# Performance work log

Hardware: AMD Instinct MI355X
Metric: run time of the kernel (lower is better)

The kernel has to match this reference:

```python
import jax, jax.numpy as jnp
import numpy as np

D_MODEL = 1024
N_HEADS = 16
D_HEAD = D_MODEL // N_HEADS


def setup_inputs() -> dict:
    key = jax.random.key(0)
    kx, kq, kk, kv, ko = jax.random.split(key, 5)
    s = 1.0 / np.sqrt(D_MODEL)  # ~ nn.Linear init scale
    return {
        "x": jax.random.normal(kx, (2, 2048, D_MODEL), dtype=jnp.float32),
        "Wq": jax.random.uniform(kq, (D_MODEL, D_MODEL), jnp.float32, -s, s),
        "Wk": jax.random.uniform(kk, (D_MODEL, D_MODEL), jnp.float32, -s, s),
        "Wv": jax.random.uniform(kv, (D_MODEL, D_MODEL), jnp.float32, -s, s),
        "Wo": jax.random.uniform(ko, (D_MODEL, D_MODEL), jnp.float32, -s, s),
    }


def reference(x, Wq, Wk, Wv, Wo):
    B, T, D = x.shape
    H, Dh = N_HEADS, D_HEAD
    # nn.Linear computes x @ W.T; project then split heads -> [B,H,T,Dh]
    q = (x @ Wq.T).reshape(B, T, H, Dh).transpose(0, 2, 1, 3)
    k = (x @ Wk.T).reshape(B, T, H, Dh).transpose(0, 2, 1, 3)
    v = (x @ Wv.T).reshape(B, T, H, Dh).transpose(0, 2, 1, 3)
    att = jnp.einsum("bhqd,bhkd->bhqk", q, k) / jnp.sqrt(jnp.float32(Dh))
    causal = jnp.tril(jnp.ones((T, T), dtype=bool))  # True = keep
    att = jnp.where(causal[None, None], att, -jnp.inf)
    w = jax.nn.softmax(att, axis=-1)
    out = jnp.einsum("bhqk,bhkd->bhqd", w, v)
    out = out.transpose(0, 2, 1, 3).reshape(B, T, D)
    return out @ Wo.T
```

## Files before the change

### kernel.cpp

```cpp
#include <hip/hip_runtime.h>
#include <hip/hip_bf16.h>

typedef __bf16 bf16;
typedef __bf16 bf16x4 __attribute__((ext_vector_type(4)));
typedef __bf16 bf16x8 __attribute__((ext_vector_type(8)));
typedef float  f32x4  __attribute__((ext_vector_type(4)));

#define DEV static __device__ __forceinline__

DEV void gload_lds16(const void* g, void* l) {
  __builtin_amdgcn_global_load_lds((const __attribute__((address_space(1))) void*)g,
                                   (__attribute__((address_space(3))) void*)l, 16, 0, 0);
}

DEV f32x4 mfma16(bf16x8 a, bf16x8 b, f32x4 c) {
  return __builtin_amdgcn_mfma_f32_16x16x32_bf16(a, b, c, 0, 0, 0);
}

__global__ void convert_all(const float* __restrict__ x,
                            const float* __restrict__ wq, const float* __restrict__ wk,
                            const float* __restrict__ wv, const float* __restrict__ wo,
                            bf16* __restrict__ xb,
                            bf16* __restrict__ wqb, bf16* __restrict__ wkb,
                            bf16* __restrict__ wvb, bf16* __restrict__ wob) {
  const int NX = 4194304;
  const int NW = 1048576;
  const int total4 = (NX + 4 * NW) / 4;
  for (int i = blockIdx.x * blockDim.x + threadIdx.x; i < total4;
       i += gridDim.x * blockDim.x) {
    int e = i * 4;
    const float* src; bf16* dst; int off;
    if (e < NX) { src = x; dst = xb; off = e; }
    else {
      int r = e - NX; int w = r >> 20; off = r & (NW - 1);
      src = (w == 0) ? wq : (w == 1) ? wk : (w == 2) ? wv : wo;
      dst = (w == 0) ? wqb : (w == 1) ? wkb : (w == 2) ? wvb : wob;
    }
    float4 v = *(const float4*)(src + off);
    bf16x4 o; o[0] = (bf16)v.x; o[1] = (bf16)v.y; o[2] = (bf16)v.z; o[3] = (bf16)v.w;
    *(bf16x4*)(dst + off) = o;
  }
}

__global__ __launch_bounds__(256) void gemm_qkv(const bf16* __restrict__ xb,
                                                const bf16* __restrict__ Wq_,
                                                const bf16* __restrict__ Wk_,
                                                const bf16* __restrict__ Wv_,
                                                bf16* __restrict__ Qg,
                                                bf16* __restrict__ Kg,
                                                bf16* __restrict__ Vtg) {
  const int z = blockIdx.z;
  const bf16* A  = (z == 2) ? Wv_ : xb;
  const bf16* Bw = (z == 0) ? Wq_ : (z == 1) ? Wk_ : xb;
  const int K = 1024;
  __shared__ bf16 As[128 * 32];
  __shared__ bf16 Bs[128 * 32];
  const int tid = threadIdx.x, w = tid >> 6, l = tid & 63;
  const int row0 = (z == 2 ? blockIdx.y : blockIdx.x) * 128;
  const int col0 = (z == 2 ? blockIdx.x : blockIdx.y) * 128;
  const int wr = (w >> 1) * 64, wc = (w & 1) * 64;
  const int lr = l & 15, lg = l >> 4;
  const int srow = l >> 2, scol = (l & 3) * 8;
  f32x4 acc[4][4] = {};

  for (int kt = 0; kt < 32; ++kt) {
    const int k0 = kt * 32;
#pragma unroll
    for (int i = 0; i < 2; ++i) {
      const int chunk = w * 2 + i;
      gload_lds16(A  + (row0 + chunk * 16 + srow) * K + k0 + scol, &As[chunk * 512]);
      gload_lds16(Bw + (col0 + chunk * 16 + srow) * K + k0 + scol, &Bs[chunk * 512]);
    }
    __syncthreads();
    bf16x8 af[4], bfr[4];
#pragma unroll
    for (int m = 0; m < 4; ++m) af[m]  = *(const bf16x8*)&As[(wr + m * 16 + lr) * 32 + lg * 8];
#pragma unroll
    for (int n = 0; n < 4; ++n) bfr[n] = *(const bf16x8*)&Bs[(wc + n * 16 + lr) * 32 + lg * 8];
#pragma unroll
    for (int m = 0; m < 4; ++m)
#pragma unroll
      for (int n = 0; n < 4; ++n)
        acc[m][n] = mfma16(af[m], bfr[n], acc[m][n]);
    __syncthreads();
  }

  if (z == 2) {
#pragma unroll
    for (int m = 0; m < 4; ++m)
#pragma unroll
      for (int n = 0; n < 4; ++n)
#pragma unroll
        for (int e = 0; e < 4; ++e) {
          const int rr = row0 + wr + m * 16 + lg * 4 + e;
          const int cc = col0 + wc + n * 16 + lr;
          const int h = rr >> 6, dh = rr & 63;
          const int b = cc >> 11, t = cc & 2047;
          Vtg[(((size_t)(b * 16 + h) * 64) + dh) * 2048 + t] = (bf16)acc[m][n][e];
        }
  } else {
    const float scl = (z == 0) ? 0.18033688011112042f : 1.0f;
    bf16* out = (z == 0) ? Qg : Kg;
#pragma unroll
    for (int m = 0; m < 4; ++m)
#pragma unroll
      for (int n = 0; n < 4; ++n)
#pragma unroll
        for (int e = 0; e < 4; ++e) {
          const int r = row0 + wr + m * 16 + lg * 4 + e;
          const int c = col0 + wc + n * 16 + lr;
          const int b = r >> 11, t = r & 2047;
          const int h = c >> 6,  dh = c & 63;
          out[(((size_t)(b * 16 + h) * 2048) + t) * 64 + dh] = (bf16)(acc[m][n][e] * scl);
        }
  }
}

__global__ __launch_bounds__(256) void attn(const bf16* __restrict__ Qg,
                                            const bf16* __restrict__ Kg,
                                            const bf16* __restrict__ Vtg,
                                            bf16* __restrict__ Obt) {
  const int bh = blockIdx.y;
  const int x  = blockIdx.x;
  const int tid = threadIdx.x, w = tid >> 6, l = tid & 63;
  const int lr = l & 15, lg = l >> 4;
  __shared__ bf16 Ks[2][4096];
  __shared__ bf16 Vs[2][4096];
  __shared__ bf16 Ps[4][1024];
  const size_t base = (size_t)bh * 2048 * 64;
  const char* kbase = (const char*)(Kg + base);
  const char* vbase = (const char*)(Vtg + base);

  const int rA0 = x * 64 + w * 16;
  const int rB0 = (31 - x) * 64 + w * 16;

  bf16x8 qA[2], qB[2];
  {
    const bf16* qp = Qg + base + (size_t)(rA0 + lr) * 64;
    qA[0] = *(const bf16x8*)(qp + lg * 8);
    qA[1] = *(const bf16x8*)(qp + 32 + lg * 8);
    const bf16* qq = Qg + base + (size_t)(rB0 + lr) * 64;
    qB[0] = *(const bf16x8*)(qq + lg * 8);
    qB[1] = *(const bf16x8*)(qq + 32 + lg * 8);
  }
  f32x4 oA[4] = {}, oB[4] = {};
  f32x4 lA = {}, lB = {};

  bf16x8 ones;
#pragma unroll
  for (int j = 0; j < 8; ++j) ones[j] = (bf16)1.0f;

  const int cxor = lr & 7;

  auto stage = [&](int kt, int buf) {
#pragma unroll
    for (int i = 0; i < 2; ++i) {
      const int p = (w * 2 + i) * 1024 + l * 16;
      const int sw = p ^ (((p >> 7) & 7) << 4);
      gload_lds16(kbase + (size_t)kt * 8192 + sw, &Ks[buf][(w * 2 + i) * 512]);
      const int vrow = p >> 7;
      const int vcol = (p & 127) ^ (((p >> 7) & 7) << 4);
      gload_lds16(vbase + (size_t)vrow * 4096 + kt * 128 + vcol,
                  &Vs[buf][(w * 2 + i) * 512]);
    }
  };

  auto computeTile = [&](int kt, int buf, int myrow0, bf16x8 (&qf)[2],
                         f32x4 (&acco)[4], f32x4& lacc) {
    const int k0 = kt * 64;
    const bool full = (k0 + 63 <= myrow0);
    f32x4 accs[4] = {};
    __builtin_amdgcn_s_setprio(1);
#pragma unroll
    for (int n = 0; n < 4; ++n) {
      const int r = n * 16 + lr;
      bf16x8 kf0 = *(const bf16x8*)&Ks[buf][(r * 128 + ((lg ^ cxor) << 4)) / 2];
      bf16x8 kf1 = *(const bf16x8*)&Ks[buf][(r * 128 + (((4 + lg) ^ cxor) << 4)) / 2];
      accs[n] = mfma16(kf0, qf[0], accs[n]);
      accs[n] = mfma16(kf1, qf[1], accs[n]);
    }
    __builtin_amdgcn_s_setprio(0);
    if (!full) {
      const int q = myrow0 + lr;
#pragma unroll
      for (int n = 0; n < 4; ++n) {
        const int keyb = k0 + n * 16 + lg * 4;
#pragma unroll
        for (int e = 0; e < 4; ++e)
          if (keyb + e > q) accs[n][e] = -__builtin_inff();
      }
    }
#pragma unroll
    for (int n = 0; n < 4; ++n)
#pragma unroll
      for (int e = 0; e < 4; ++e) accs[n][e] = exp2f(accs[n][e]);
#pragma unroll
    for (int n = 0; n < 4; ++n) {
      bf16x4 p4;
#pragma unroll
      for (int e = 0; e < 4; ++e) p4[e] = (bf16)accs[n][e];
      const int off = (lr * 128 + (n * 16 + lg * 4) * 2) ^ ((lr & 7) << 4);
      *(bf16x4*)((char*)Ps[w] + off) = p4;
    }
    __builtin_amdgcn_s_setprio(1);
#pragma unroll
    for (int c = 0; c < 2; ++c) {
      bf16x8 pf = *(const bf16x8*)((char*)Ps[w] +
                    (lr * 128 + (((c * 4 + lg) ^ cxor) << 4)));
      lacc = mfma16(pf, ones, lacc);
#pragma unroll
      for (int n = 0; n < 4; ++n) {
        const int r = n * 16 + lr;
        bf16x8 vf = *(const bf16x8*)&Vs[buf][(r * 128 + (((c * 4 + lg) ^ cxor) << 4)) / 2];
        acco[n] = mfma16(pf, vf, acco[n]);
      }
    }
    __builtin_amdgcn_s_setprio(0);
  };

  const int nkt = 32 - x;
  stage(0, 0);
  int cur = 0;
  for (int kt = 0; kt < nkt; ++kt) {
    __syncthreads();
    if (kt + 1 < nkt) stage(kt + 1, cur ^ 1);
    if (kt <= x)
      computeTile(kt, cur, rA0, qA, oA, lA);
    computeTile(kt, cur, rB0, qB, oB, lB);
    cur ^= 1;
  }

  const int b = bh >> 4, h = bh & 15;
  f32x4 invA, invB;
#pragma unroll
  for (int e = 0; e < 4; ++e) {
    invA[e] = __builtin_amdgcn_rcpf(lA[e]);
    invB[e] = __builtin_amdgcn_rcpf(lB[e]);
  }
#pragma unroll
  for (int n = 0; n < 4; ++n)
#pragma unroll
    for (int e = 0; e < 4; ++e) {
      const int rA = rA0 + lg * 4 + e;
      Obt[((size_t)(b * 2048 + rA)) * 1024 + h * 64 + n * 16 + lr] = (bf16)(oA[n][e] * invA[e]);
      const int rB = rB0 + lg * 4 + e;
      Obt[((size_t)(b * 2048 + rB)) * 1024 + h * 64 + n * 16 + lr] = (bf16)(oB[n][e] * invB[e]);
    }
}

__global__ __launch_bounds__(256) void gemm_out(const bf16* __restrict__ A,
                                                const bf16* __restrict__ Bw,
                                                float* __restrict__ Cout) {
  const int K = 1024;
  __shared__ bf16 As[128 * 32];
  __shared__ bf16 Bs[128 * 32];
  const int tid = threadIdx.x, w = tid >> 6, l = tid & 63;
  const int row0 = blockIdx.x * 128, col0 = blockIdx.y * 128;
  const int wr = (w >> 1) * 64, wc = (w & 1) * 64;
  const int lr = l & 15, lg = l >> 4;
  const int srow = l >> 2, scol = (l & 3) * 8;
  f32x4 acc[4][4] = {};

  for (int kt = 0; kt < 32; ++kt) {
    const int k0 = kt * 32;
#pragma unroll
    for (int i = 0; i < 2; ++i) {
      const int chunk = w * 2 + i;
      gload_lds16(A  + (row0 + chunk * 16 + srow) * K + k0 + scol, &As[chunk * 512]);
      gload_lds16(Bw + (col0 + chunk * 16 + srow) * K + k0 + scol, &Bs[chunk * 512]);
    }
    __syncthreads();
    bf16x8 af[4], bfr[4];
#pragma unroll
    for (int m = 0; m < 4; ++m) af[m]  = *(const bf16x8*)&As[(wr + m * 16 + lr) * 32 + lg * 8];
#pragma unroll
    for (int n = 0; n < 4; ++n) bfr[n] = *(const bf16x8*)&Bs[(wc + n * 16 + lr) * 32 + lg * 8];
#pragma unroll
    for (int m = 0; m < 4; ++m)
#pragma unroll
      for (int n = 0; n < 4; ++n)
        acc[m][n] = mfma16(af[m], bfr[n], acc[m][n]);
    __syncthreads();
  }

#pragma unroll
  for (int m = 0; m < 4; ++m)
#pragma unroll
    for (int n = 0; n < 4; ++n)
#pragma unroll
      for (int e = 0; e < 4; ++e) {
        const int r = row0 + wr + m * 16 + lg * 4 + e;
        const int c = col0 + wc + n * 16 + lr;
        Cout[(size_t)r * 1024 + c] = acc[m][n][e];
      }
}

extern "C" void kernel_launch(void* const* d_in, const int* in_sizes, int n_in,
                              void* d_out, int out_size, void* d_ws, size_t ws_size,
                              hipStream_t stream) {
  const float* x  = (const float*)d_in[0];
  const float* wq = (const float*)d_in[1];
  const float* wk = (const float*)d_in[2];
  const float* wv = (const float*)d_in[3];
  const float* wo = (const float*)d_in[4];
  float* out = (float*)d_out;

  bf16* xb  = (bf16*)d_ws;
  bf16* wqb = xb  + 4194304;
  bf16* wkb = wqb + 1048576;
  bf16* wvb = wkb + 1048576;
  bf16* wob = wvb + 1048576;
  bf16* Qg  = wob + 1048576;
  bf16* Kg  = Qg  + 4194304;
  bf16* Vtg = Kg  + 4194304;
  bf16* Obt = Vtg + 4194304;

  convert_all<<<2048, 256, 0, stream>>>(x, wq, wk, wv, wo, xb, wqb, wkb, wvb, wob);
  gemm_qkv<<<dim3(32, 8, 3), 256, 0, stream>>>(xb, wqb, wkb, wvb, Qg, Kg, Vtg);
  attn<<<dim3(16, 32), 256, 0, stream>>>(Qg, Kg, Vtg, Obt);
  gemm_out<<<dim3(32, 8), 256, 0, stream>>>(Obt, wob, out);
}
```

Before: 118.9 us.

## Double-buffer LDS tiles in QKV and output projection GEMMs

Both GEMM kernels now keep two LDS buffers per operand. The next K-tile's global-to-LDS async loads are issued right after the barrier, before the MFMA work on the current tile, and the trailing barrier is dropped. The goal is to hide global load latency behind matrix math. This doubles LDS use per block, which may lower occupancy, and the compiler may still insert conservative waits on the async LDS loads that limit the overlap.

```diff
diff --git a/kernel.cpp b/kernel.cpp
--- a/kernel.cpp
+++ b/kernel.cpp
@@ -53,8 +53,8 @@
   const bf16* A  = (z == 2) ? Wv_ : xb;
   const bf16* Bw = (z == 0) ? Wq_ : (z == 1) ? Wk_ : xb;
   const int K = 1024;
-  __shared__ bf16 As[128 * 32];
-  __shared__ bf16 Bs[128 * 32];
+  __shared__ bf16 As[2][128 * 32];
+  __shared__ bf16 Bs[2][128 * 32];
   const int tid = threadIdx.x, w = tid >> 6, l = tid & 63;
   const int row0 = (z == 2 ? blockIdx.y : blockIdx.x) * 128;
   const int col0 = (z == 2 ? blockIdx.x : blockIdx.y) * 128;
@@ -63,26 +63,32 @@
   const int srow = l >> 2, scol = (l & 3) * 8;
   f32x4 acc[4][4] = {};
 
-  for (int kt = 0; kt < 32; ++kt) {
+  auto stage = [&](int kt, int buf) {
     const int k0 = kt * 32;
 #pragma unroll
     for (int i = 0; i < 2; ++i) {
       const int chunk = w * 2 + i;
-      gload_lds16(A  + (row0 + chunk * 16 + srow) * K + k0 + scol, &As[chunk * 512]);
-      gload_lds16(Bw + (col0 + chunk * 16 + srow) * K + k0 + scol, &Bs[chunk * 512]);
-    }
+      gload_lds16(A  + (row0 + chunk * 16 + srow) * K + k0 + scol, &As[buf][chunk * 512]);
+      gload_lds16(Bw + (col0 + chunk * 16 + srow) * K + k0 + scol, &Bs[buf][chunk * 512]);
+    }
+  };
+
+  stage(0, 0);
+  int cur = 0;
+  for (int kt = 0; kt < 32; ++kt) {
     __syncthreads();
+    if (kt + 1 < 32) stage(kt + 1, cur ^ 1);
     bf16x8 af[4], bfr[4];
 #pragma unroll
-    for (int m = 0; m < 4; ++m) af[m]  = *(const bf16x8*)&As[(wr + m * 16 + lr) * 32 + lg * 8];
-#pragma unroll
-    for (int n = 0; n < 4; ++n) bfr[n] = *(const bf16x8*)&Bs[(wc + n * 16 + lr) * 32 + lg * 8];
+    for (int m = 0; m < 4; ++m) af[m]  = *(const bf16x8*)&As[cur][(wr + m * 16 + lr) * 32 + lg * 8];
+#pragma unroll
+    for (int n = 0; n < 4; ++n) bfr[n] = *(const bf16x8*)&Bs[cur][(wc + n * 16 + lr) * 32 + lg * 8];
 #pragma unroll
     for (int m = 0; m < 4; ++m)
 #pragma unroll
       for (int n = 0; n < 4; ++n)
         acc[m][n] = mfma16(af[m], bfr[n], acc[m][n]);
-    __syncthreads();
+    cur ^= 1;
   }
 
   if (z == 2) {
@@ -252,8 +258,8 @@
                                                 const bf16* __restrict__ Bw,
                                                 float* __restrict__ Cout) {
   const int K = 1024;
-  __shared__ bf16 As[128 * 32];
-  __shared__ bf16 Bs[128 * 32];
+  __shared__ bf16 As[2][128 * 32];
+  __shared__ bf16 Bs[2][128 * 32];
   const int tid = threadIdx.x, w = tid >> 6, l = tid & 63;
   const int row0 = blockIdx.x * 128, col0 = blockIdx.y * 128;
   const int wr = (w >> 1) * 64, wc = (w & 1) * 64;
@@ -261,26 +267,32 @@
   const int srow = l >> 2, scol = (l & 3) * 8;
   f32x4 acc[4][4] = {};
 
-  for (int kt = 0; kt < 32; ++kt) {
+  auto stage = [&](int kt, int buf) {
     const int k0 = kt * 32;
 #pragma unroll
     for (int i = 0; i < 2; ++i) {
       const int chunk = w * 2 + i;
-      gload_lds16(A  + (row0 + chunk * 16 + srow) * K + k0 + scol, &As[chunk * 512]);
-      gload_lds16(Bw + (col0 + chunk * 16 + srow) * K + k0 + scol, &Bs[chunk * 512]);
-    }
+      gload_lds16(A  + (row0 + chunk * 16 + srow) * K + k0 + scol, &As[buf][chunk * 512]);
+      gload_lds16(Bw + (col0 + chunk * 16 + srow) * K + k0 + scol, &Bs[buf][chunk * 512]);
+    }
+  };
+
+  stage(0, 0);
+  int cur = 0;
+  for (int kt = 0; kt < 32; ++kt) {
     __syncthreads();
+    if (kt + 1 < 32) stage(kt + 1, cur ^ 1);
     bf16x8 af[4], bfr[4];
 #pragma unroll
-    for (int m = 0; m < 4; ++m) af[m]  = *(const bf16x8*)&As[(wr + m * 16 + lr) * 32 + lg * 8];
-#pragma unroll
-    for (int n = 0; n < 4; ++n) bfr[n] = *(const bf16x8*)&Bs[(wc + n * 16 + lr) * 32 + lg * 8];
+    for (int m = 0; m < 4; ++m) af[m]  = *(const bf16x8*)&As[cur][(wr + m * 16 + lr) * 32 + lg * 8];
+#pragma unroll
+    for (int n = 0; n < 4; ++n) bfr[n] = *(const bf16x8*)&Bs[cur][(wc + n * 16 + lr) * 32 + lg * 8];
 #pragma unroll
     for (int m = 0; m < 4; ++m)
 #pragma unroll
       for (int n = 0; n < 4; ++n)
         acc[m][n] = mfma16(af[m], bfr[n], acc[m][n]);
-    __syncthreads();
+    cur ^= 1;
   }
 
 #pragma unroll
```

Result: slower. 125.2 us (+5.3%).
